# Kernel tuning notes

Measured on AMD Instinct MI355X. Metric: run time of the kernel, lower is better.

## Reference

```python
import jax, jax.numpy as jnp
import numpy as np

START_IDX = 1  # PAD_IDX = 0, END_IDX = 2 (unused in teacher-forcing path)
B, N, F = 16, 49, 1024
H, E, V = 1024, 1024, 15000
S, W = 5, 12


def setup_inputs() -> dict:
    key = jax.random.key(0)
    ks = jax.random.split(key, 16)
    def w(k, shape, s=0.02):
        return jax.random.normal(k, shape, dtype=jnp.float32) * s
    emb = w(ks[0], (V, E)).at[0].set(0.0)  # padding_idx = 0
    return dict(
        features=jax.random.normal(ks[1], (B, N, F), dtype=jnp.float32),
        reports=jax.random.randint(ks[2], (B, S, W), 0, V),
        attn_w1=w(ks[3], (F + H, H)), attn_b1=jnp.zeros((H,), jnp.float32),
        attn_w2=w(ks[4], (H, 1)), attn_b2=jnp.zeros((1,), jnp.float32),
        s_wih=w(ks[5], (4 * H, F)), s_whh=w(ks[6], (4 * H, H)),
        s_bih=jnp.zeros((4 * H,), jnp.float32), s_bhh=jnp.zeros((4 * H,), jnp.float32),
        stop_w=w(ks[7], (H, 1)), stop_b=jnp.zeros((1,), jnp.float32),
        emb=emb,
        w_wih=w(ks[8], (4 * H, E)), w_whh=w(ks[9], (4 * H, H)),
        w_bih=jnp.zeros((4 * H,), jnp.float32), w_bhh=jnp.zeros((4 * H,), jnp.float32),
        fc_w=w(ks[10], (H, V)), fc_b=jnp.zeros((V,), jnp.float32),
    )


def _lstm_cell(x, h, c, wih, whh, bih, bhh):
    # PyTorch LSTMCell: gates ordered i, f, g, o
    gates = x @ wih.T + h @ whh.T + (bih + bhh)
    i, f, g, o = jnp.split(gates, 4, axis=-1)
    c = jax.nn.sigmoid(f) * c + jax.nn.sigmoid(i) * jnp.tanh(g)
    h = jax.nn.sigmoid(o) * jnp.tanh(c)
    return h, c


def _attention(features, h, w1, b1, w2, b2):
    # features [B,N,F], h [B,H] -> additive 2-layer attention over N locations
    b, n, _ = features.shape
    hcat = jnp.broadcast_to(h[:, None, :], (b, n, h.shape[-1]))
    x = jnp.concatenate([features, hcat], axis=-1)           # [B,N,F+H]
    e = (jnp.tanh(x @ w1 + b1) @ w2 + b2)[..., 0]            # [B,N]
    scores = jax.nn.softmax(e, axis=-1)
    att = jnp.einsum('bn,bnf->bf', scores, features)          # [B,F]
    return att, scores


def _forward(features, reports, attn_w1, attn_b1, attn_w2, attn_b2,
             s_wih, s_whh, s_bih, s_bhh, stop_w, stop_b, emb,
             w_wih, w_whh, w_bih, w_bhh, fc_w, fc_b):
    bsz = features.shape[0]
    h0 = jnp.zeros((bsz, s_whh.shape[-1]), features.dtype)
    att0, _ = _attention(features, h0, attn_w1, attn_b1, attn_w2, attn_b2)
    start_emb = jnp.broadcast_to(emb[START_IDX][None, :], (bsz, emb.shape[-1]))

    def sentence_step(carry, reports_i):   # reports_i: [W, B] teacher-forcing tokens
        h, c, att = carry
        h, c = _lstm_cell(att, h, c, s_wih, s_whh, s_bih, s_bhh)
        czero = jnp.zeros_like(h)

        def word_step(wc, idx):
            hw, cw, inp = wc
            hw, cw = _lstm_cell(inp, hw, cw, w_wih, w_whh, w_bih, w_bhh)
            pred = hw @ fc_w + fc_b                           # [B,V]
            return (hw, cw, emb[idx]), pred

        # word LSTM initialized with h=topic, c=0; first input = <start> embedding
        _, preds = jax.lax.scan(word_step, (h, czero, start_emb), reports_i)  # [W,B,V]
        stop = jax.nn.sigmoid(h @ stop_w + stop_b)[:, 0]      # [B]
        att, scores = _attention(features, h, attn_w1, attn_b1, attn_w2, attn_b2)
        return (h, c, att), (preds, stop, scores)

    reports_sw = jnp.transpose(reports, (1, 2, 0))            # [S,W,B]
    _, (seq, stops, scores) = jax.lax.scan(sentence_step, (h0, h0, att0), reports_sw)
    seq_out = jnp.transpose(seq, (2, 0, 1, 3))                # [B,S,W,V]
    stops_out = jnp.transpose(stops, (1, 0))                  # [B,S]
    scores_out = jnp.transpose(scores, (1, 0, 2))             # [B,S,N]
    return seq_out, stops_out, scores_out


def reference(features, reports, attn_w1, attn_b1, attn_w2, attn_b2,
              s_wih, s_whh, s_bih, s_bhh, stop_w, stop_b, emb,
              w_wih, w_whh, w_bih, w_bhh, fc_w, fc_b):
    return _forward(features, reports, attn_w1, attn_b1, attn_w2, attn_b2,
                    s_wih, s_whh, s_bih, s_bhh, stop_w, stop_b, emb,
                    w_wih, w_whh, w_bih, w_bhh, fc_w, fc_b)
```

## Files before the change

kernel.cpp:

```cpp
#include <hip/hip_runtime.h>
#include <hip/hip_bf16.h>

#define B_  16
#define S_  5
#define W_  12
#define NL_ 49
#define H_  1024
#define V_  15000
#define SEQ_N   14400000
#define STOP_N  80
#define OUT_STOP (SEQ_N)
#define OUT_SCORE (SEQ_N + STOP_N)

typedef __attribute__((ext_vector_type(8))) short     short8;
typedef __attribute__((ext_vector_type(4))) float     f32x4;
typedef __attribute__((ext_vector_type(4))) unsigned int u32x4;
typedef __attribute__((ext_vector_type(4))) unsigned short us4;

#define OFF_FCWT   0ull
#define OFF_WWHHP  30720000ull
#define OFF_WWIHP  39108608ull
#define OFF_WSCATP 47497216ull
#define OFF_W1AT   64274432ull
#define OFF_W1BT   66371584ull
#define OFF_FBF    68468736ull
#define OFF_XIN    70074368ull
#define OFF_PF     72040448ull
#define OFF_XW     75251712ull
#define OFF_HBALL  90980352ull
#define OFF_HWBF0  92946432ull
#define OFF_HWBF1  93110272ull
#define OFF_ACAT1  93274112ull
#define OFF_H      93339648ull
#define OFF_EVAL   93405184ull
#define OFF_ACAT0  93408384ull
#define OFF_C      93473920ull
#define OFF_CW     93539456ull
#define OFF_HPROJ  93867136ull
#define WS_TOTAL   93932672ull
#define ZERO_BASE  OFF_ACAT0
#define ZERO_BYTES (524288ull)

__device__ __forceinline__ unsigned short f2bf(float x){
  unsigned u = __float_as_uint(x);
  u += 0x7fffu + ((u >> 16) & 1u);
  return (unsigned short)(u >> 16);
}
__device__ __forceinline__ float sigm(float x){ return 1.f/(1.f+expf(-x)); }

typedef __attribute__((address_space(3))) unsigned int  as3_u32;
typedef __attribute__((address_space(1))) const unsigned int as1_u32;

__device__ __forceinline__ void gl16(const void* g, void* l){
  __builtin_amdgcn_global_load_lds((as1_u32*)g, (as3_u32*)l, 16, 0, 0);
}

template<int ROWS,int CH,int NW>
__device__ __forceinline__ void stage_swz(const unsigned short* __restrict__ gbase, int grs,
                                          unsigned short* lds, int wid, int lane,
                                          int r0, int rmax){
  constexpr int RPI = 64/CH;
  constexpr int NISS = ROWS/RPI;
  const int r_in = lane / CH;
  const int cbp  = lane % CH;
  #pragma unroll
  for (int it = wid; it < NISS; it += NW){
    int rl = it*RPI + r_in;
    int gr = r0 + rl; gr = gr < rmax ? gr : rmax-1;
    int cb = cbp ^ (rl & 7);
    gl16(gbase + (size_t)gr*grs + cb*8, lds + it*RPI*CH*8);
  }
}

__device__ __forceinline__ void transp64(const float* __restrict__ src, int sld,
                                         int rb, int cb, int Cc,
                                         unsigned short* __restrict__ dst, int dld,
                                         float (*t)[65])
{
  const int tx = threadIdx.x & 15, ty = threadIdx.x >> 4;
  #pragma unroll
  for (int ii = 0; ii < 4; ii++){
    int r = ty + ii*16;
    int c = cb + tx*4;
    const float* s = src + (size_t)(rb + r)*sld + c;
    f32x4 v;
    if (c + 4 <= Cc) v = *(const f32x4*)s;
    else {
      v[0] = (c   < Cc) ? s[0] : 0.f;
      v[1] = (c+1 < Cc) ? s[1] : 0.f;
      v[2] = (c+2 < Cc) ? s[2] : 0.f;
      v[3] = (c+3 < Cc) ? s[3] : 0.f;
    }
    t[r][tx*4+0]=v[0]; t[r][tx*4+1]=v[1]; t[r][tx*4+2]=v[2]; t[r][tx*4+3]=v[3];
  }
  __syncthreads();
  #pragma unroll
  for (int ii = 0; ii < 4; ii++){
    int c = ty + ii*16;
    if (cb + c < Cc){
      int r4 = tx*4;
      us4 o; o[0]=f2bf(t[r4][c]); o[1]=f2bf(t[r4+1][c]); o[2]=f2bf(t[r4+2][c]); o[3]=f2bf(t[r4+3][c]);
      *(us4*)(dst + (size_t)(cb + c)*dld + rb + r4) = o;
    }
  }
}

__device__ __forceinline__ void cvt_gate_blk(const float* __restrict__ src,
                                             unsigned short* __restrict__ dst,
                                             int blk, int dld, int doff){
  int idx = (blk*256 + threadIdx.x)*4;
  int n = idx >> 10, cc = idx & 1023;
  int gate = (n >> 4) & 3, j = ((n >> 6) << 4) | (n & 15);
  f32x4 v = *(const f32x4*)(src + ((size_t)(gate*1024 + j) << 10) + cc);
  us4 o; o[0]=f2bf(v[0]); o[1]=f2bf(v[1]); o[2]=f2bf(v[2]); o[3]=f2bf(v[3]);
  *(us4*)(dst + (size_t)n*dld + doff + cc) = o;
}

#define P0 784
#define P1 (P0+4096)
#define P2 (P1+4096)
#define P3 (P2+4096)
#define P4 (P3+4096)
#define P5 (P4+960)
#define P6 (P5+512)
#define P7 (P6+3760)
#define P8 (P7+128)

__global__ void k_prep(const float* __restrict__ features,
                       const float* __restrict__ w_whh, const float* __restrict__ w_wih,
                       const float* __restrict__ s_wih, const float* __restrict__ s_whh,
                       const float* __restrict__ emb, const int* __restrict__ reports,
                       const float* __restrict__ attn_w1, const float* __restrict__ fc_w,
                       unsigned short* __restrict__ FBF, unsigned short* __restrict__ WWHHP,
                       unsigned short* __restrict__ WWIHP, unsigned short* __restrict__ WSCATP,
                       unsigned short* __restrict__ XIN,
                       unsigned short* __restrict__ W1AT, unsigned short* __restrict__ W1BT,
                       unsigned short* __restrict__ FCWT, char* __restrict__ zbase)
{
  __shared__ float t[64][65];
  int bx = blockIdx.x;
  if (bx < P0){
    int idx = (bx*256 + threadIdx.x)*4;
    f32x4 v = *(const f32x4*)(features + idx);
    us4 o; o[0]=f2bf(v[0]); o[1]=f2bf(v[1]); o[2]=f2bf(v[2]); o[3]=f2bf(v[3]);
    *(us4*)(FBF + idx) = o;
  } else if (bx < P1){
    cvt_gate_blk(w_whh, WWHHP, bx - P0, 1024, 0);
  } else if (bx < P2){
    cvt_gate_blk(w_wih, WWIHP, bx - P1, 1024, 0);
  } else if (bx < P3){
    cvt_gate_blk(s_wih, WSCATP, bx - P2, 2048, 0);
  } else if (bx < P4){
    cvt_gate_blk(s_whh, WSCATP, bx - P3, 2048, 1024);
  } else if (bx < P5){
    int m = bx - P4;
    int w = m / 80, r = m % 80, s = r >> 4, b = r & 15;
    int tok = (w == 0) ? 1 : reports[b*60 + s*12 + (w-1)];
    const float* src = emb + ((size_t)tok << 10);
    int k = threadIdx.x * 4;
    f32x4 v = *(const f32x4*)(src + k);
    us4 o; o[0]=f2bf(v[0]); o[1]=f2bf(v[1]); o[2]=f2bf(v[2]); o[3]=f2bf(v[3]);
    *(us4*)(XIN + (size_t)m*1024 + k) = o;
  } else if (bx < P6){
    int idx = bx - P5;
    int z = idx >> 8, rem = idx & 255;
    int rb = (rem & 15)*64, cb = (rem >> 4)*64;
    transp64(attn_w1 + (size_t)z*1024*1024, 1024, rb, cb, 1024, z ? W1BT : W1AT, 1024, t);
  } else if (bx < P7){
    int idx = bx - P6;
    int rb = (idx & 15)*64, cb = (idx >> 4)*64;
    transp64(fc_w, V_, rb, cb, V_, FCWT, 1024, t);
  } else {
    int idx = bx - P7;
    *(u32x4*)(zbase + ((size_t)idx*256 + threadIdx.x)*16) = (u32x4){0u,0u,0u,0u};
  }
}

template<int BM,int BN,int BK,int WM,int WN,int EPI>
__global__ void k_gemm(const unsigned short* __restrict__ A, int lda,
                       const unsigned short* __restrict__ Bt, int ldb,
                       float* __restrict__ C, int ldc,
                       const float* __restrict__ bias,
                       int M, int N, int K)
{
  constexpr int NWV = WM*WN;
  constexpr int CH = BK/8;
  __shared__ __align__(16) unsigned short As[BM*BK];
  __shared__ __align__(16) unsigned short Bs[BN*BK];
  const int n0 = blockIdx.x * BN, m0 = blockIdx.y * BM;
  if (n0 >= N) return;
  const int tid  = threadIdx.x;
  const int lane = tid & 63;
  const int wave = tid >> 6;
  constexpr int WROWS = BM/WM, WCOLS = BN/WN;
  constexpr int FM = WROWS/16, FN = WCOLS/16;
  const int wm = wave / WN, wn = wave % WN;
  const int g = lane >> 4, fr = lane & 15;
  const int sx = fr & 7;

  f32x4 acc[FM][FN];
  #pragma unroll
  for (int a=0;a<FM;a++)
    #pragma unroll
    for (int b=0;b<FN;b++) acc[a][b] = (f32x4){0.f,0.f,0.f,0.f};

  for (int k0 = 0; k0 < K; k0 += BK) {
    if (k0) __syncthreads();
    stage_swz<BM,CH,NWV>(A + k0, lda, As, wave, lane, m0, M);
    stage_swz<BN,CH,NWV>(Bt + k0, ldb, Bs, wave, lane, n0, N);
    __syncthreads();
    #pragma unroll
    for (int kk = 0; kk < BK; kk += 32) {
      const int so = ((kk/8 + g) ^ sx) * 8;
      short8 af[FM], bt[FN];
      #pragma unroll
      for (int fm=0; fm<FM; fm++)
        af[fm] = *(const short8*)(As + (wm*WROWS + fm*16 + fr)*BK + so);
      #pragma unroll
      for (int fn=0; fn<FN; fn++)
        bt[fn] = *(const short8*)(Bs + (wn*WCOLS + fn*16 + fr)*BK + so);
      #pragma unroll
      for (int fm=0; fm<FM; fm++)
        #pragma unroll
        for (int fn=0; fn<FN; fn++)
          acc[fm][fn] = __builtin_amdgcn_mfma_f32_16x16x32_bf16(af[fm], bt[fn], acc[fm][fn], 0, 0, 0);
    }
  }

  #pragma unroll
  for (int fm=0; fm<FM; fm++)
    #pragma unroll
    for (int fn=0; fn<FN; fn++)
      #pragma unroll
      for (int j=0; j<4; j++){
        int m = m0 + wm*WROWS + fm*16 + g*4 + j;
        int n = n0 + wn*WCOLS + fn*16 + fr;
        if (m < M && n < N) {
          float v = acc[fm][fn][j];
          if (EPI == 1 || EPI == 2) v += bias[n];
          if (EPI == 2) {
            int b = m & 15, s = (m >> 4) % 5, w = m / 80;
            __builtin_nontemporal_store(v, &C[(size_t)((b*5 + s)*12 + w)*V_ + n]);
          } else if (EPI == 3) {
            __builtin_nontemporal_store(v, &C[(size_t)m*ldc + n]);
          } else {
            C[(size_t)m*ldc + n] = v;
          }
        }
      }
}

template<int BM,int BN,int BK,int WN,int SENT>
__global__ void k_gemm_cell(const unsigned short* __restrict__ A, int lda,
                            const unsigned short* __restrict__ Bt, int ldb,
                            const float* __restrict__ Xg, int ldx,
                            const float* __restrict__ bih, const float* __restrict__ bhh,
                            float* __restrict__ cst,
                            unsigned short* __restrict__ h1, int ldh1,
                            unsigned short* __restrict__ h2,
                            float* __restrict__ hf,
                            int M, int K)
{
  constexpr int CH = BK/8;
  __shared__ __align__(16) unsigned short As[BM*BK];
  __shared__ __align__(16) unsigned short Bs[BN*BK];
  const int tid  = threadIdx.x;
  const int lane = tid & 63;
  const int wn   = tid >> 6;
  const int n0 = blockIdx.x * BN, m0 = blockIdx.y * BM;
  const int g = lane >> 4, fr = lane & 15;
  const int sx = fr & 7;

  f32x4 acc[4];
  #pragma unroll
  for (int b=0;b<4;b++) acc[b] = (f32x4){0.f,0.f,0.f,0.f};

  for (int k0 = 0; k0 < K; k0 += BK) {
    if (k0) __syncthreads();
    stage_swz<BM,CH,WN>(A + k0, lda, As, wn, lane, m0, M);
    stage_swz<BN,CH,WN>(Bt + k0, ldb, Bs, wn, lane, n0, 4096);
    __syncthreads();
    #pragma unroll
    for (int kk = 0; kk < BK; kk += 32) {
      const int so = ((kk/8 + g) ^ sx) * 8;
      short8 af = *(const short8*)(As + fr*BK + so);
      #pragma unroll
      for (int fn=0; fn<4; fn++){
        short8 bt = *(const short8*)(Bs + (wn*64 + fn*16 + fr)*BK + so);
        acc[fn] = __builtin_amdgcn_mfma_f32_16x16x32_bf16(af, bt, acc[fn], 0, 0, 0);
      }
    }
  }

  const int nb = n0 + wn*64 + fr;
  const int j  = ((n0 + wn*64) >> 2) + fr;
  const float b0 = bih[j]        + bhh[j];
  const float b1 = bih[1024 + j] + bhh[1024 + j];
  const float b2 = bih[2048 + j] + bhh[2048 + j];
  const float b3 = bih[3072 + j] + bhh[3072 + j];
  #pragma unroll
  for (int jj=0; jj<4; jj++){
    int m = m0 + g*4 + jj;
    if (m < M){
      float gi = acc[0][jj] + b0;
      float gf = acc[1][jj] + b1;
      float gg = acc[2][jj] + b2;
      float go = acc[3][jj] + b3;
      if (!SENT){
        const float* xg = Xg + (size_t)m*ldx + nb;
        gi += xg[0]; gf += xg[16]; gg += xg[32]; go += xg[48];
      }
      float cn = sigm(gf)*cst[m*1024 + j] + sigm(gi)*tanhf(gg);
      float hn = sigm(go)*tanhf(cn);
      cst[m*1024 + j] = cn;
      unsigned short hb = f2bf(hn);
      h1[(size_t)m*ldh1 + j] = hb;
      h2[(size_t)m*1024 + j] = hb;
      if (SENT) hf[m*1024 + j] = hn;
    }
  }
}

__global__ void k_attn_e(const float* __restrict__ PF, const float* __restrict__ hproj,
                         const float* __restrict__ w2, float* __restrict__ evals)
{
  const int bn = blockIdx.x;
  const int b  = bn / NL_;
  const int tid = threadIdx.x;
  __shared__ float red[4];
  const float* pf = PF + ((size_t)bn << 10);
  const float* hp = hproj + (b << 10);
  int k = tid * 4;
  f32x4 a = *(const f32x4*)(pf + k);
  f32x4 hh = *(const f32x4*)(hp + k);
  f32x4 w = *(const f32x4*)(w2 + k);
  float p = tanhf(a[0]+hh[0])*w[0] + tanhf(a[1]+hh[1])*w[1]
          + tanhf(a[2]+hh[2])*w[2] + tanhf(a[3]+hh[3])*w[3];
  #pragma unroll
  for (int o = 32; o; o >>= 1) p += __shfl_down(p, o, 64);
  if ((tid & 63) == 0) red[tid >> 6] = p;
  __syncthreads();
  if (tid == 0) evals[bn] = red[0] + red[1] + red[2] + red[3];
}

template<int INIT>
__global__ void k_attn_fin(const float* __restrict__ evals, const float* __restrict__ features,
                           const float* __restrict__ h, const float* __restrict__ stop_w,
                           const float* __restrict__ stop_b,
                           unsigned short* __restrict__ Acat, float* __restrict__ outp, int s)
{
  const int b = blockIdx.x, tid = threadIdx.x;
  __shared__ float scs[64];
  __shared__ float red[4];
  if (tid < 64){
    float e = (tid < NL_) ? evals[b*NL_ + tid] : -1e30f;
    float mx = e;
    #pragma unroll
    for (int o = 32; o; o >>= 1) mx = fmaxf(mx, __shfl_xor(mx, o, 64));
    float ex = (tid < NL_) ? expf(e - mx) : 0.f;
    float dn = ex;
    #pragma unroll
    for (int o = 32; o; o >>= 1) dn += __shfl_xor(dn, o, 64);
    float sc = ex / dn;
    if (tid < NL_){
      scs[tid] = sc;
      if (!INIT) outp[OUT_SCORE + (b*5 + s)*NL_ + tid] = sc;
    }
  }
  __syncthreads();
  {
    int f0 = tid * 4;
    f32x4 a = (f32x4){0.f,0.f,0.f,0.f};
    const float* fb = features + (((size_t)b*NL_) << 10) + f0;
    #pragma unroll 7
    for (int n = 0; n < NL_; n++){
      f32x4 v = *(const f32x4*)(fb + ((size_t)n << 10));
      float sc = scs[n];
      a[0] += sc*v[0]; a[1] += sc*v[1]; a[2] += sc*v[2]; a[3] += sc*v[3];
    }
    us4 o4; o4[0]=f2bf(a[0]); o4[1]=f2bf(a[1]); o4[2]=f2bf(a[2]); o4[3]=f2bf(a[3]);
    *(us4*)(Acat + b*2048 + f0) = o4;
  }
  if (!INIT){
    int k = tid * 4;
    f32x4 hv = *(const f32x4*)(h + (b << 10) + k);
    f32x4 sw = *(const f32x4*)(stop_w + k);
    float p = hv[0]*sw[0] + hv[1]*sw[1] + hv[2]*sw[2] + hv[3]*sw[3];
    #pragma unroll
    for (int o = 32; o; o >>= 1) p += __shfl_down(p, o, 64);
    if ((tid & 63) == 0) red[tid >> 6] = p;
    __syncthreads();
    if (tid == 0) outp[OUT_STOP + b*5 + s] = sigm(red[0]+red[1]+red[2]+red[3] + stop_b[0]);
  }
}

extern "C" void kernel_launch(void* const* d_in, const int* in_sizes, int n_in,
                              void* d_out, int out_size, void* d_ws, size_t ws_size,
                              hipStream_t stream)
{
  const float* features = (const float*)d_in[0];
  const int*   reports  = (const int*)d_in[1];
  const float* attn_w1  = (const float*)d_in[2];
  const float* attn_b1  = (const float*)d_in[3];
  const float* attn_w2  = (const float*)d_in[4];
  const float* s_wih    = (const float*)d_in[6];
  const float* s_whh    = (const float*)d_in[7];
  const float* s_bih    = (const float*)d_in[8];
  const float* s_bhh    = (const float*)d_in[9];
  const float* stop_w   = (const float*)d_in[10];
  const float* stop_b   = (const float*)d_in[11];
  const float* emb      = (const float*)d_in[12];
  const float* w_wih    = (const float*)d_in[13];
  const float* w_whh    = (const float*)d_in[14];
  const float* w_bih    = (const float*)d_in[15];
  const float* w_bhh    = (const float*)d_in[16];
  const float* fc_w     = (const float*)d_in[17];
  const float* fc_b     = (const float*)d_in[18];
  float* out = (float*)d_out;
  char*  ws  = (char*)d_ws;
  if (ws_size < WS_TOTAL) return;

  unsigned short* FCWT   = (unsigned short*)(ws + OFF_FCWT);
  unsigned short* WWHHP  = (unsigned short*)(ws + OFF_WWHHP);
  unsigned short* WWIHP  = (unsigned short*)(ws + OFF_WWIHP);
  unsigned short* WSCATP = (unsigned short*)(ws + OFF_WSCATP);
  unsigned short* W1AT   = (unsigned short*)(ws + OFF_W1AT);
  unsigned short* W1BT   = (unsigned short*)(ws + OFF_W1BT);
  unsigned short* FBF    = (unsigned short*)(ws + OFF_FBF);
  unsigned short* XIN    = (unsigned short*)(ws + OFF_XIN);
  float*          PF     = (float*)(ws + OFF_PF);
  float*          XW     = (float*)(ws + OFF_XW);
  unsigned short* HBALL  = (unsigned short*)(ws + OFF_HBALL);
  unsigned short* HW0    = (unsigned short*)(ws + OFF_HWBF0);
  unsigned short* HW1    = (unsigned short*)(ws + OFF_HWBF1);
  unsigned short* ACAT0  = (unsigned short*)(ws + OFF_ACAT0);
  unsigned short* ACAT1  = (unsigned short*)(ws + OFF_ACAT1);
  float*          Hst    = (float*)(ws + OFF_H);
  float*          Cst    = (float*)(ws + OFF_C);
  float*          CW     = (float*)(ws + OFF_CW);
  float*          HPROJ  = (float*)(ws + OFF_HPROJ);
  float*          EVAL   = (float*)(ws + OFF_EVAL);

  k_prep<<<P8, 256, 0, stream>>>(features, w_whh, w_wih, s_wih, s_whh, emb, reports,
                                 attn_w1, fc_w,
                                 FBF, WWHHP, WWIHP, WSCATP, XIN, W1AT, W1BT, FCWT,
                                 ws + ZERO_BASE);

  k_gemm<64,64,128,2,2,1><<<dim3(16,13), 256, 0, stream>>>(FBF,1024, W1AT,1024, PF,1024, attn_b1, 784,1024,1024);
  k_gemm<64,128,128,2,2,3><<<dim3(32,15), 256, 0, stream>>>(XIN,1024, WWIHP,1024, XW,4096, nullptr, 960,4096,1024);

  k_attn_e<<<784, 256, 0, stream>>>(PF, HPROJ, attn_w2, EVAL);
  k_attn_fin<1><<<16, 256, 0, stream>>>(EVAL, features, Hst, stop_w, stop_b, ACAT0, out, 0);

  unsigned short* ACS[2] = {ACAT0, ACAT1};
  for (int s = 0; s < S_; s++){
    unsigned short* cur = ACS[s & 1];
    unsigned short* nxt = ACS[(s + 1) & 1];
    k_gemm_cell<16,128,128,2,1><<<dim3(32,1), 128, 0, stream>>>(
        cur, 2048, WSCATP, 2048, nullptr, 0, s_bih, s_bhh, Cst,
        nxt + 1024, 2048, HW0 + s*16*1024, Hst, 16, 2048);
    k_gemm<16,64,256,1,4,0><<<dim3(16,1), 256, 0, stream>>>(
        nxt + 1024, 2048, W1BT, 1024, HPROJ, 1024, nullptr, 16, 1024, 1024);
    k_attn_e<<<784, 256, 0, stream>>>(PF, HPROJ, attn_w2, EVAL);
    k_attn_fin<0><<<16, 256, 0, stream>>>(EVAL, features, Hst, stop_w, stop_b, nxt, out, s);
  }

  unsigned short* HW[2] = {HW0, HW1};
  for (int w = 0; w < W_; w++){
    k_gemm_cell<16,128,128,2,0><<<dim3(32,5), 128, 0, stream>>>(
        HW[w & 1], 1024, WWHHP, 1024, XW + (size_t)w*80*4096, 4096, w_bih, w_bhh, CW,
        HW[(w + 1) & 1], 1024, HBALL + (size_t)w*80*1024, nullptr, 80, 1024);
  }

  k_gemm<128,128,64,2,2,2><<<dim3(120,8), 256, 0, stream>>>(HBALL,1024, FCWT,1024, out,V_, fc_b, 960,15000,1024);
}
```

Before: 529.6 us.

## Consolidate prep kernel into grid-stride blocks and shrink final FC GEMM tile

The weight/feature conversion part of k_prep now runs as a fixed pool of 1280 blocks that grid-stride over all elements, instead of one block per 1024 elements. Each transpose block now handles four 64x64 tiles, and each zeroing block clears eight chunks, which cuts the prep launch from about 21k blocks to about 2.4k. The final vocabulary projection GEMM switches from 128x128 to 64x128 tiles (120x15 grid), giving more workgroups to fill the CUs. The trade-off is less per-block reuse in the output GEMM and extra loop and __syncthreads overhead in the prep kernel.

Measured after the change: 526.8 us. No clear change (-0.5%).

```diff
diff --git a/kernel.cpp b/kernel.cpp
--- a/kernel.cpp
+++ b/kernel.cpp
@@ -105,26 +105,26 @@
   }
 }
 
-__device__ __forceinline__ void cvt_gate_blk(const float* __restrict__ src,
-                                             unsigned short* __restrict__ dst,
-                                             int blk, int dld, int doff){
-  int idx = (blk*256 + threadIdx.x)*4;
-  int n = idx >> 10, cc = idx & 1023;
+#define U0 200704u
+#define U1 (U0+1048576u)
+#define U2 (U1+1048576u)
+#define U3 (U2+1048576u)
+#define U4 (U3+1048576u)
+#define U5 (U4+245760u)
+#define NCVT_BLK 1280
+#define NTR_BLK  1068
+#define NZ_BLK   16
+#define NPREP    (NCVT_BLK + NTR_BLK + NZ_BLK)
+
+__device__ __forceinline__ void cvt_gate_unit(const float* __restrict__ src,
+                                              unsigned short* __restrict__ dst,
+                                              unsigned e, int dld, int doff){
+  int n = e >> 8, cc = (e & 255)*4;
   int gate = (n >> 4) & 3, j = ((n >> 6) << 4) | (n & 15);
   f32x4 v = *(const f32x4*)(src + ((size_t)(gate*1024 + j) << 10) + cc);
   us4 o; o[0]=f2bf(v[0]); o[1]=f2bf(v[1]); o[2]=f2bf(v[2]); o[3]=f2bf(v[3]);
   *(us4*)(dst + (size_t)n*dld + doff + cc) = o;
 }
-
-#define P0 784
-#define P1 (P0+4096)
-#define P2 (P1+4096)
-#define P3 (P2+4096)
-#define P4 (P3+4096)
-#define P5 (P4+960)
-#define P6 (P5+512)
-#define P7 (P6+3760)
-#define P8 (P7+128)
 
 __global__ void k_prep(const float* __restrict__ features,
                        const float* __restrict__ w_whh, const float* __restrict__ w_wih,
@@ -139,40 +139,54 @@
 {
   __shared__ float t[64][65];
   int bx = blockIdx.x;
-  if (bx < P0){
-    int idx = (bx*256 + threadIdx.x)*4;
-    f32x4 v = *(const f32x4*)(features + idx);
-    us4 o; o[0]=f2bf(v[0]); o[1]=f2bf(v[1]); o[2]=f2bf(v[2]); o[3]=f2bf(v[3]);
-    *(us4*)(FBF + idx) = o;
-  } else if (bx < P1){
-    cvt_gate_blk(w_whh, WWHHP, bx - P0, 1024, 0);
-  } else if (bx < P2){
-    cvt_gate_blk(w_wih, WWIHP, bx - P1, 1024, 0);
-  } else if (bx < P3){
-    cvt_gate_blk(s_wih, WSCATP, bx - P2, 2048, 0);
-  } else if (bx < P4){
-    cvt_gate_blk(s_whh, WSCATP, bx - P3, 2048, 1024);
-  } else if (bx < P5){
-    int m = bx - P4;
-    int w = m / 80, r = m % 80, s = r >> 4, b = r & 15;
-    int tok = (w == 0) ? 1 : reports[b*60 + s*12 + (w-1)];
-    const float* src = emb + ((size_t)tok << 10);
-    int k = threadIdx.x * 4;
-    f32x4 v = *(const f32x4*)(src + k);
-    us4 o; o[0]=f2bf(v[0]); o[1]=f2bf(v[1]); o[2]=f2bf(v[2]); o[3]=f2bf(v[3]);
-    *(us4*)(XIN + (size_t)m*1024 + k) = o;
-  } else if (bx < P6){
-    int idx = bx - P5;
-    int z = idx >> 8, rem = idx & 255;
-    int rb = (rem & 15)*64, cb = (rem >> 4)*64;
-    transp64(attn_w1 + (size_t)z*1024*1024, 1024, rb, cb, 1024, z ? W1BT : W1AT, 1024, t);
-  } else if (bx < P7){
-    int idx = bx - P6;
-    int rb = (idx & 15)*64, cb = (idx >> 4)*64;
-    transp64(fc_w, V_, rb, cb, V_, FCWT, 1024, t);
+  if (bx < NCVT_BLK){
+    for (unsigned u = bx*256u + threadIdx.x; u < U5; u += NCVT_BLK*256u){
+      if (u < U0){
+        int idx = u*4;
+        f32x4 v = *(const f32x4*)(features + idx);
+        us4 o; o[0]=f2bf(v[0]); o[1]=f2bf(v[1]); o[2]=f2bf(v[2]); o[3]=f2bf(v[3]);
+        *(us4*)(FBF + idx) = o;
+      } else if (u < U1){
+        cvt_gate_unit(w_whh, WWHHP, u - U0, 1024, 0);
+      } else if (u < U2){
+        cvt_gate_unit(w_wih, WWIHP, u - U1, 1024, 0);
+      } else if (u < U3){
+        cvt_gate_unit(s_wih, WSCATP, u - U2, 2048, 0);
+      } else if (u < U4){
+        cvt_gate_unit(s_whh, WSCATP, u - U3, 2048, 1024);
+      } else {
+        unsigned e = u - U4;
+        int m = e >> 8, k = (e & 255)*4;
+        int w = m / 80, r = m % 80, s = r >> 4, b = r & 15;
+        int tok = (w == 0) ? 1 : reports[b*60 + s*12 + (w-1)];
+        f32x4 v = *(const f32x4*)(emb + ((size_t)tok << 10) + k);
+        us4 o; o[0]=f2bf(v[0]); o[1]=f2bf(v[1]); o[2]=f2bf(v[2]); o[3]=f2bf(v[3]);
+        *(us4*)(XIN + (size_t)m*1024 + k) = o;
+      }
+    }
+  } else if (bx < NCVT_BLK + NTR_BLK){
+    int base = (bx - NCVT_BLK)*4;
+    #pragma unroll
+    for (int bt = 0; bt < 4; bt++){
+      if (bt) __syncthreads();
+      int tile = base + bt;
+      if (tile < 512){
+        int z = tile >> 8, rem = tile & 255;
+        int rb = (rem & 15)*64, cb = (rem >> 4)*64;
+        transp64(attn_w1 + (size_t)z*1024*1024, 1024, rb, cb, 1024, z ? W1BT : W1AT, 1024, t);
+      } else {
+        int ft = tile - 512;
+        int rb = (ft & 15)*64, cb = (ft >> 4)*64;
+        transp64(fc_w, V_, rb, cb, V_, FCWT, 1024, t);
+      }
+    }
   } else {
-    int idx = bx - P7;
-    *(u32x4*)(zbase + ((size_t)idx*256 + threadIdx.x)*16) = (u32x4){0u,0u,0u,0u};
+    int idx = bx - (NCVT_BLK + NTR_BLK);
+    #pragma unroll
+    for (int it = 0; it < 8; it++){
+      size_t off = ((size_t)(idx + it*NZ_BLK))*4096 + threadIdx.x*16;
+      *(u32x4*)(zbase + off) = (u32x4){0u,0u,0u,0u};
+    }
   }
 }
 
@@ -441,10 +455,10 @@
   float*          HPROJ  = (float*)(ws + OFF_HPROJ);
   float*          EVAL   = (float*)(ws + OFF_EVAL);
 
-  k_prep<<<P8, 256, 0, stream>>>(features, w_whh, w_wih, s_wih, s_whh, emb, reports,
-                                 attn_w1, fc_w,
-                                 FBF, WWHHP, WWIHP, WSCATP, XIN, W1AT, W1BT, FCWT,
-                                 ws + ZERO_BASE);
+  k_prep<<<NPREP, 256, 0, stream>>>(features, w_whh, w_wih, s_wih, s_whh, emb, reports,
+                                    attn_w1, fc_w,
+                                    FBF, WWHHP, WWIHP, WSCATP, XIN, W1AT, W1BT, FCWT,
+                                    ws + ZERO_BASE);
 
   k_gemm<64,64,128,2,2,1><<<dim3(16,13), 256, 0, stream>>>(FBF,1024, W1AT,1024, PF,1024, attn_b1, 784,1024,1024);
   k_gemm<64,128,128,2,2,3><<<dim3(32,15), 256, 0, stream>>>(XIN,1024, WWIHP,1024, XW,4096, nullptr, 960,4096,1024);
@@ -472,5 +486,5 @@
         HW[(w + 1) & 1], 1024, HBALL + (size_t)w*80*1024, nullptr, 80, 1024);
   }
 
-  k_gemm<128,128,64,2,2,2><<<dim3(120,8), 256, 0, stream>>>(HBALL,1024, FCWT,1024, out,V_, fc_b, 960,15000,1024);
-}
+  k_gemm<64,128,64,2,2,2><<<dim3(120,15), 256, 0, stream>>>(HBALL,1024, FCWT,1024, out,V_, fc_b, 960,15000,1024);
+}
```
